# Performance work log

Measured on AMD Instinct MI355X. Metric: run time of the kernel, lower is better.

The kernel has to match this reference:

```python
import jax, jax.numpy as jnp
import numpy as np

N = 50000
E = 800000
D_IN = 128
D_H = 128
N_CLASSES = 40
N_HIDDEN = 2


def _gcn_norm(edge_index, num_nodes):
    # Add self loops, compute symmetric normalization D^-1/2 (A+I) D^-1/2
    loops = jnp.arange(num_nodes, dtype=edge_index.dtype)
    src = jnp.concatenate([edge_index[0], loops])
    dst = jnp.concatenate([edge_index[1], loops])
    deg = jax.ops.segment_sum(jnp.ones_like(src, dtype=jnp.float32), dst,
                              num_segments=num_nodes)
    dinv = jnp.where(deg > 0, jax.lax.rsqrt(jnp.maximum(deg, 1.0)), 0.0)
    norm = dinv[src] * dinv[dst]  # [E+N]
    return src, dst, norm


def _gcn_conv(x, src, dst, norm, W, b):
    h = x @ W                          # [N, d_out] transform first (PyG order)
    msg = h[src] * norm[:, None]       # gather + scale, [E+N, d_out]
    out = jax.ops.segment_sum(msg, dst, num_segments=x.shape[0])
    return out + b


def setup_inputs() -> dict:
    key = jax.random.key(0)
    ks = jax.random.split(key, 8)
    x = jax.random.normal(ks[0], (N, D_IN), dtype=jnp.float32)
    edge_index = jax.random.randint(ks[1], (2, E), 0, N, dtype=jnp.int64)
    s = 1.0 / np.sqrt(D_IN)
    W1 = jax.random.uniform(ks[2], (D_IN, D_H), minval=-s, maxval=s, dtype=jnp.float32)
    b1 = jnp.zeros((D_H,), dtype=jnp.float32)
    sh = 1.0 / np.sqrt(D_H)
    Wh = jax.random.uniform(ks[3], (N_HIDDEN, D_H, D_H), minval=-sh, maxval=sh, dtype=jnp.float32)
    bh = jnp.zeros((N_HIDDEN, D_H), dtype=jnp.float32)
    Wf = jax.random.uniform(ks[4], (D_H, N_CLASSES), minval=-sh, maxval=sh, dtype=jnp.float32)
    bf = jnp.zeros((N_CLASSES,), dtype=jnp.float32)
    return {"x": x, "edge_index": edge_index, "W1": W1, "b1": b1,
            "Wh": Wh, "bh": bh, "Wf": Wf, "bf": bf}


def reference(x, edge_index, W1, b1, Wh, bh, Wf, bf):
    src, dst, norm = _gcn_norm(edge_index, x.shape[0])
    h = jax.nn.relu(_gcn_conv(x, src, dst, norm, W1, b1))
    for i in range(Wh.shape[0]):  # small fixed layer count
        h = jax.nn.relu(_gcn_conv(h, src, dst, norm, Wh[i], bh[i]))
    # extra relu in original forward is a no-op after relu above
    return h @ Wf + bf
```

## Files before the change

### kernel.cpp

```cpp
#include <hip/hip_runtime.h>

#define D 128
#define NC 40

typedef __attribute__((ext_vector_type(8))) short short8v;
typedef __attribute__((ext_vector_type(4))) float f32x4;

__device__ __forceinline__ unsigned short f2bf(float f) {
    unsigned u = __float_as_uint(f);
    u += 0x7fff + ((u >> 16) & 1);
    return (unsigned short)(u >> 16);
}
__device__ __forceinline__ float bf2f(unsigned short h) {
    return __uint_as_float(((unsigned)h) << 16);
}

__device__ __forceinline__ int load_idx(const int* ei, long long pos, int is64) {
    return is64 ? ei[pos * 2] : ei[pos];
}

__device__ __forceinline__ int detect64(const int* __restrict__ ei) {
    int lane = threadIdx.x & 63;
    int hi = ei[lane * 2 + 1];
    return __any(hi != 0) ? 0 : 1;
}


__global__ void count_convert_kernel(const int* __restrict__ ei, int* __restrict__ deg,
                                     int E, int EB,
                                     const float* __restrict__ W1, const float* __restrict__ Wh,
                                     const float* __restrict__ Wf,
                                     unsigned short* __restrict__ Wc1, unsigned short* __restrict__ Wch0,
                                     unsigned short* __restrict__ Wch1, unsigned short* __restrict__ Wcf) {
    if (blockIdx.x < EB) {
        int is64 = detect64(ei);
        int e = blockIdx.x * 256 + threadIdx.x;
        if (e < E) {
            int d = load_idx(ei, (long long)E + e, is64);
            atomicAdd(&deg[d], 1);
        }
    } else {
        int idx = (blockIdx.x - EB) * 256 + threadIdx.x;
        if (idx < 49152) {
            int which = idx >> 14;
            int j = idx & 16383;
            int nn = j >> 7, k = j & 127;
            const float* W = (which == 0) ? W1 : (which == 1) ? Wh : Wh + 16384;
            unsigned short* o = (which == 0) ? Wc1 : (which == 1) ? Wch0 : Wch1;
            float v = W[k * 128 + nn];
            unsigned short h = f2bf(v);
            o[j] = h;
            o[16384 + j] = f2bf(v - bf2f(h));
        } else if (idx < 49152 + 6144) {
            int j = idx - 49152;
            int nn = j >> 7, k = j & 127;
            float v = (nn < NC) ? Wf[k * NC + nn] : 0.f;
            unsigned short h = f2bf(v);
            Wcf[j] = h;
            Wcf[6144 + j] = f2bf(v - bf2f(h));
        }
    }
}

__global__ void scan1_kernel(const int* __restrict__ deg, int* __restrict__ bsum, int m) {
    int i = blockIdx.x * 512 + threadIdx.x;
    int v = (i < m) ? deg[i] : 0;
    #pragma unroll
    for (int off = 32; off; off >>= 1) v += __shfl_down(v, off, 64);
    __shared__ int ws[8];
    if ((threadIdx.x & 63) == 0) ws[threadIdx.x >> 6] = v;
    __syncthreads();
    if (threadIdx.x == 0) {
        int s = 0;
        #pragma unroll
        for (int j = 0; j < 8; ++j) s += ws[j];
        bsum[blockIdx.x] = s;
    }
}

__global__ void scan3_kernel(const int* __restrict__ deg, const int* __restrict__ bsum,
                             int* __restrict__ rowptr, int* __restrict__ fill,
                             float* __restrict__ dinv, int n, int E, int nb) {
    int t = threadIdx.x;
    int lane = t & 63, w = t >> 6;
    int pv = (t < nb && t < (int)blockIdx.x) ? bsum[t] : 0;
    int rs = pv;
    #pragma unroll
    for (int off = 32; off; off >>= 1) rs += __shfl_down(rs, off, 64);
    __shared__ int red[8];
    if (lane == 0) red[w] = rs;
    __syncthreads();
    int base = 0;
    #pragma unroll
    for (int j = 0; j < 8; ++j) base += red[j];
    __syncthreads();

    int i = blockIdx.x * 512 + t;
    int v = (i < n) ? deg[i] : 0;
    int s = v;
    #pragma unroll
    for (int off = 1; off < 64; off <<= 1) {
        int x = __shfl_up(s, off, 64);
        if (lane >= off) s += x;
    }
    __shared__ int wsum[8];
    if (lane == 63) wsum[w] = s;
    __syncthreads();
    int wbase = 0;
    #pragma unroll
    for (int j = 0; j < 8; ++j) if (j < w) wbase += wsum[j];
    int excl = base + wbase + s - v;
    if (i < n) {
        rowptr[i] = excl;
        fill[i]   = excl;
        dinv[i]   = rsqrtf((float)(v + 1));
    }
    if (i == 0) rowptr[n] = E;
}

__global__ void scatter_kernel(const int* __restrict__ ei, int* __restrict__ fill,
                               const float* __restrict__ dinv, int2* __restrict__ col2, int E) {
    int is64 = detect64(ei);
    int e = blockIdx.x * 256 + threadIdx.x;
    if (e >= E) return;
    int s = load_idx(ei, (long long)e, is64);
    int d = load_idx(ei, (long long)E + e, is64);
    int pos = atomicAdd(&fill[d], 1);
    col2[pos] = make_int2(s, __float_as_int(dinv[s]));
}

__launch_bounds__(256)
__global__ void fused_wave_kernel(const float4* __restrict__ h4,
                                  const unsigned short* __restrict__ Wcvt,
                                  const float* __restrict__ bias,
                                  const float* __restrict__ dinv,
                                  const int* __restrict__ rowptr, const int2* __restrict__ col2,
                                  float* __restrict__ out, int n) {
    __shared__ unsigned short S[4][2][2][128];
    int t = threadIdx.x;
    int wv = t >> 6, l = t & 63;
    int p = l >> 5, li = l & 31;
    int kg = l >> 4, lr = l & 15;
    int base = blockIdx.x * 64 + wv * 16;
    if (base >= n) return;

    short8v fAh[4], fAl[4];
    #pragma unroll
    for (int ks = 0; ks < 4; ++ks) {
        fAh[ks] = (short8v){0,0,0,0,0,0,0,0};
        fAl[ks] = (short8v){0,0,0,0,0,0,0,0};
    }

    for (int j = 0; j < 8; ++j) {
        int node = base + 2 * j + p;
        int nd = (node < n) ? node : (n - 1);
        float dn = dinv[nd];
        size_t rowbase = (size_t)nd * 32;
        float4 hv = h4[rowbase + li];
        float4 acc;
        acc.x = hv.x * dn; acc.y = hv.y * dn; acc.z = hv.z * dn; acc.w = hv.w * dn;
        int e = rowptr[nd], e1 = rowptr[nd + 1];
        for (; e + 8 <= e1; e += 8) {
            int2 c[8];
            #pragma unroll
            for (int q = 0; q < 8; ++q) c[q] = col2[e + q];
            float4 v[8];
            #pragma unroll
            for (int q = 0; q < 8; ++q) v[q] = h4[(size_t)c[q].x * 32 + li];
            #pragma unroll
            for (int q = 0; q < 8; ++q) {
                float ds = __int_as_float(c[q].y);
                acc.x += v[q].x * ds; acc.y += v[q].y * ds;
                acc.z += v[q].z * ds; acc.w += v[q].w * ds;
            }
        }
        for (; e + 4 <= e1; e += 4) {
            int2 c[4];
            #pragma unroll
            for (int q = 0; q < 4; ++q) c[q] = col2[e + q];
            float4 v[4];
            #pragma unroll
            for (int q = 0; q < 4; ++q) v[q] = h4[(size_t)c[q].x * 32 + li];
            #pragma unroll
            for (int q = 0; q < 4; ++q) {
                float ds = __int_as_float(c[q].y);
                acc.x += v[q].x * ds; acc.y += v[q].y * ds;
                acc.z += v[q].z * ds; acc.w += v[q].w * ds;
            }
        }
        for (; e < e1; ++e) {
            int2 c = col2[e];
            float ds = __int_as_float(c.y);
            float4 v = h4[(size_t)c.x * 32 + li];
            acc.x += v.x * ds; acc.y += v.y * ds; acc.z += v.z * ds; acc.w += v.w * ds;
        }
        acc.x *= dn; acc.y *= dn; acc.z *= dn; acc.w *= dn;

        ushort4 hi, lo;
        hi.x = f2bf(acc.x); lo.x = f2bf(acc.x - bf2f(hi.x));
        hi.y = f2bf(acc.y); lo.y = f2bf(acc.y - bf2f(hi.y));
        hi.z = f2bf(acc.z); lo.z = f2bf(acc.z - bf2f(hi.z));
        hi.w = f2bf(acc.w); lo.w = f2bf(acc.w - bf2f(hi.w));
        *(ushort4*)&S[wv][0][p][li * 4] = hi;
        *(ushort4*)&S[wv][1][p][li * 4] = lo;
        __builtin_amdgcn_wave_barrier();
        if ((lr >> 1) == j) {
            int rp = lr & 1;
            #pragma unroll
            for (int ks = 0; ks < 4; ++ks) {
                fAh[ks] = *(short8v*)&S[wv][0][rp][ks * 32 + kg * 8];
                fAl[ks] = *(short8v*)&S[wv][1][rp][ks * 32 + kg * 8];
            }
        }
        __builtin_amdgcn_wave_barrier();
    }

    const unsigned short* Whi = Wcvt;
    const unsigned short* Wlo = Wcvt + 128 * 128;
    #pragma unroll
    for (int nt = 0; nt < 8; ++nt) {
        int col = nt * 16 + lr;
        short8v bh[4], bl[4];
        #pragma unroll
        for (int ks = 0; ks < 4; ++ks) {
            bh[ks] = *(const short8v*)&Whi[col * 128 + ks * 32 + kg * 8];
            bl[ks] = *(const short8v*)&Wlo[col * 128 + ks * 32 + kg * 8];
        }
        f32x4 o = (f32x4){0.f, 0.f, 0.f, 0.f};
        #pragma unroll
        for (int ks = 0; ks < 4; ++ks) {
            o = __builtin_amdgcn_mfma_f32_16x16x32_bf16(fAh[ks], bh[ks], o, 0, 0, 0);
            o = __builtin_amdgcn_mfma_f32_16x16x32_bf16(fAh[ks], bl[ks], o, 0, 0, 0);
            o = __builtin_amdgcn_mfma_f32_16x16x32_bf16(fAl[ks], bh[ks], o, 0, 0, 0);
        }
        float bv = bias[col];
        #pragma unroll
        for (int r = 0; r < 4; ++r) {
            int row = base + kg * 4 + r;
            if (row < n) out[(size_t)row * 128 + col] = fmaxf(o[r] + bv, 0.f);
        }
    }
}

__launch_bounds__(256)
__global__ void final_mfma_kernel(const float* __restrict__ A, const unsigned short* __restrict__ Wcvt,
                                  const float* __restrict__ bf, float* __restrict__ C, int M) {
    __shared__ unsigned short Ah[64 * 128];
    __shared__ unsigned short Al[64 * 128];
    int t = threadIdx.x;
    int l = t & 63, w = t >> 6;
    int lr = l & 15, lh = l >> 4;

    const unsigned short* Whi = Wcvt;
    const unsigned short* Wlo = Wcvt + 48 * 128;
    short8v bhi[3][4], blo[3][4];
    #pragma unroll
    for (int nt = 0; nt < 3; ++nt) {
        int n = nt * 16 + lr;
        #pragma unroll
        for (int ks = 0; ks < 4; ++ks) {
            bhi[nt][ks] = *(const short8v*)&Whi[n * 128 + ks * 32 + lh * 8];
            blo[nt][ks] = *(const short8v*)&Wlo[n * 128 + ks * 32 + lh * 8];
        }
    }

    int row0 = blockIdx.x * 64;
    #pragma unroll
    for (int c = 0; c < 4; ++c) {
        int chunk = c * 256 + t;
        int r  = chunk >> 4;
        int kc = chunk & 15;
        int gr = row0 + r; if (gr >= M) gr = M - 1;
        float4 a0 = *(const float4*)&A[(size_t)gr * 128 + kc * 8];
        float4 a1 = *(const float4*)&A[(size_t)gr * 128 + kc * 8 + 4];
        float av[8] = {a0.x, a0.y, a0.z, a0.w, a1.x, a1.y, a1.z, a1.w};
        short8v hv, lv;
        #pragma unroll
        for (int j = 0; j < 8; ++j) {
            unsigned short hi = f2bf(av[j]);
            hv[j] = (short)hi;
            lv[j] = (short)f2bf(av[j] - bf2f(hi));
        }
        int off = (r << 8) + ((kc << 4) ^ ((r & 7) << 4));
        *(short8v*)((char*)Ah + off) = hv;
        *(short8v*)((char*)Al + off) = lv;
    }
    __syncthreads();

    f32x4 acc[3];
    #pragma unroll
    for (int nt = 0; nt < 3; ++nt) acc[nt] = (f32x4){0.f, 0.f, 0.f, 0.f};
    int row = w * 16 + lr;
    #pragma unroll
    for (int ks = 0; ks < 4; ++ks) {
        int off = (row << 8) + (((ks << 6) + (lh << 4)) ^ ((row & 7) << 4));
        short8v ah = *(short8v*)((char*)Ah + off);
        short8v al = *(short8v*)((char*)Al + off);
        #pragma unroll
        for (int nt = 0; nt < 3; ++nt) {
            acc[nt] = __builtin_amdgcn_mfma_f32_16x16x32_bf16(ah, bhi[nt][ks], acc[nt], 0, 0, 0);
            acc[nt] = __builtin_amdgcn_mfma_f32_16x16x32_bf16(ah, blo[nt][ks], acc[nt], 0, 0, 0);
            acc[nt] = __builtin_amdgcn_mfma_f32_16x16x32_bf16(al, bhi[nt][ks], acc[nt], 0, 0, 0);
        }
    }
    #pragma unroll
    for (int nt = 0; nt < 3; ++nt) {
        int col = nt * 16 + lr;
        #pragma unroll
        for (int r = 0; r < 4; ++r) {
            int ro = row0 + w * 16 + lh * 4 + r;
            if (col < NC && ro < M) C[(size_t)ro * NC + col] = acc[nt][r] + bf[col];
        }
    }
}

extern "C" void kernel_launch(void* const* d_in, const int* in_sizes, int n_in,
                              void* d_out, int out_size, void* d_ws, size_t ws_size,
                              hipStream_t stream) {
    const float* x  = (const float*)d_in[0];
    const int*   ei = (const int*)d_in[1];
    const float* W1 = (const float*)d_in[2];
    const float* b1 = (const float*)d_in[3];
    const float* Wh = (const float*)d_in[4];
    const float* bh = (const float*)d_in[5];
    const float* Wf = (const float*)d_in[6];
    const float* bf = (const float*)d_in[7];
    float* out = (float*)d_out;

    int n = in_sizes[0] / D;
    int E = in_sizes[1] / 2;

    char* ws = (char*)d_ws;
    size_t off = 0;
    auto alloc = [&](size_t bytes) {
        void* p = ws + off;
        off = (off + bytes + 255) & ~(size_t)255;
        return p;
    };
    float* B0     = (float*)alloc((size_t)n * D * 4);
    float* B1     = (float*)alloc((size_t)n * D * 4);
    int*   deg    = (int*)alloc((size_t)n * 4);
    int*   rowptr = (int*)alloc((size_t)(n + 1) * 4);
    int*   fill   = (int*)alloc((size_t)n * 4);
    int2*  col2   = (int2*)alloc((size_t)E * 8);
    float* dinv   = (float*)alloc((size_t)n * 4);
    int*   bsum   = (int*)alloc(1024 * 4);
    unsigned short* Wc1  = (unsigned short*)alloc(2 * 128 * 128 * 2);
    unsigned short* Wch0 = (unsigned short*)alloc(2 * 128 * 128 * 2);
    unsigned short* Wch1 = (unsigned short*)alloc(2 * 128 * 128 * 2);
    unsigned short* Wcf  = (unsigned short*)alloc(2 * 48 * 128 * 2);

    int EB = (E + 255) / 256;
    int CB = (49152 + 6144 + 255) / 256;
    int nb = (n + 511) / 512;

    hipMemsetAsync(deg, 0, (size_t)n * 4, stream);
    count_convert_kernel<<<EB + CB, 256, 0, stream>>>(ei, deg, E, EB, W1, Wh, Wf, Wc1, Wch0, Wch1, Wcf);
    scan1_kernel<<<nb, 512, 0, stream>>>(deg, bsum, n);
    scan3_kernel<<<nb, 512, 0, stream>>>(deg, bsum, rowptr, fill, dinv, n, E, nb);
    scatter_kernel<<<EB, 256, 0, stream>>>(ei, fill, dinv, col2, E);

    int fgrid = (n + 63) / 64;

    fused_wave_kernel<<<fgrid, 256, 0, stream>>>((const float4*)x, Wc1, b1, dinv, rowptr, col2, B0, n);
    fused_wave_kernel<<<fgrid, 256, 0, stream>>>((const float4*)B0, Wch0, bh, dinv, rowptr, col2, B1, n);
    fused_wave_kernel<<<fgrid, 256, 0, stream>>>((const float4*)B1, Wch1, bh + D, dinv, rowptr, col2, B0, n);
    final_mfma_kernel<<<(n + 63) / 64, 256, 0, stream>>>(B0, Wcf, bf, out, n);
}
```

Measured before the change: 370.4 us.

## Use intra-block work stealing for GCN aggregation with shared-LDS MFMA transform

Replaces the per-wave fixed 16-node aggregation with a 512-thread block covering 32 nodes. Waves claim node pairs dynamically through a shared atomic counter, so uneven degrees are balanced across waves. Aggregated rows go into a swizzled LDS tile, and after a block barrier each of the 8 waves computes one 16-column slice of the 128x128 transform with bf16 split MFMA. The trade-off is extra atomics, a block-wide sync and smaller blocks, in exchange for better load balance and reuse of the weight fragments.

```diff
diff --git a/kernel.cpp b/kernel.cpp
--- a/kernel.cpp
+++ b/kernel.cpp
@@ -129,31 +129,30 @@
     col2[pos] = make_int2(s, __float_as_int(dinv[s]));
 }
 
-__launch_bounds__(256)
-__global__ void fused_wave_kernel(const float4* __restrict__ h4,
-                                  const unsigned short* __restrict__ Wcvt,
-                                  const float* __restrict__ bias,
-                                  const float* __restrict__ dinv,
-                                  const int* __restrict__ rowptr, const int2* __restrict__ col2,
-                                  float* __restrict__ out, int n) {
-    __shared__ unsigned short S[4][2][2][128];
+__launch_bounds__(512)
+__global__ void fused_steal_kernel(const float4* __restrict__ h4,
+                                   const unsigned short* __restrict__ Wcvt,
+                                   const float* __restrict__ bias,
+                                   const float* __restrict__ dinv,
+                                   const int* __restrict__ rowptr, const int2* __restrict__ col2,
+                                   float* __restrict__ out, int n) {
+    __shared__ unsigned short Ah[32 * 128];
+    __shared__ unsigned short Al[32 * 128];
+    __shared__ int pnodes[32];
+    __shared__ int cnt;
     int t = threadIdx.x;
     int wv = t >> 6, l = t & 63;
     int p = l >> 5, li = l & 31;
-    int kg = l >> 4, lr = l & 15;
-    int base = blockIdx.x * 64 + wv * 16;
-    if (base >= n) return;
-
-    short8v fAh[4], fAl[4];
-    #pragma unroll
-    for (int ks = 0; ks < 4; ++ks) {
-        fAh[ks] = (short8v){0,0,0,0,0,0,0,0};
-        fAl[ks] = (short8v){0,0,0,0,0,0,0,0};
-    }
-
-    for (int j = 0; j < 8; ++j) {
-        int node = base + 2 * j + p;
+    if (t == 0) cnt = 8;
+    __syncthreads();
+
+    int base = blockIdx.x * 32;
+    int pr = wv;
+    while (pr < 16) {
+        int row = 2 * pr + p;
+        int node = base + row;
         int nd = (node < n) ? node : (n - 1);
+        if (li == 0) pnodes[row] = (node < n) ? node : -1;
         float dn = dinv[nd];
         size_t rowbase = (size_t)nd * 32;
         float4 hv = h4[rowbase + li];
@@ -201,43 +200,45 @@
         hi.y = f2bf(acc.y); lo.y = f2bf(acc.y - bf2f(hi.y));
         hi.z = f2bf(acc.z); lo.z = f2bf(acc.z - bf2f(hi.z));
         hi.w = f2bf(acc.w); lo.w = f2bf(acc.w - bf2f(hi.w));
-        *(ushort4*)&S[wv][0][p][li * 4] = hi;
-        *(ushort4*)&S[wv][1][p][li * 4] = lo;
-        __builtin_amdgcn_wave_barrier();
-        if ((lr >> 1) == j) {
-            int rp = lr & 1;
-            #pragma unroll
-            for (int ks = 0; ks < 4; ++ks) {
-                fAh[ks] = *(short8v*)&S[wv][0][rp][ks * 32 + kg * 8];
-                fAl[ks] = *(short8v*)&S[wv][1][rp][ks * 32 + kg * 8];
-            }
-        }
-        __builtin_amdgcn_wave_barrier();
-    }
-
+        int off = (row << 8) + ((li << 3) ^ ((row & 7) << 4));
+        *(ushort4*)((char*)Ah + off) = hi;
+        *(ushort4*)((char*)Al + off) = lo;
+
+        int nxt;
+        if (l == 0) nxt = atomicAdd(&cnt, 1);
+        nxt = __shfl(nxt, 0);
+        pr = nxt;
+    }
+    __syncthreads();
+
+    int lr = l & 15, lh = l >> 4;
     const unsigned short* Whi = Wcvt;
     const unsigned short* Wlo = Wcvt + 128 * 128;
-    #pragma unroll
-    for (int nt = 0; nt < 8; ++nt) {
-        int col = nt * 16 + lr;
-        short8v bh[4], bl[4];
+    int col = wv * 16 + lr;
+    short8v bh[4], bl[4];
+    #pragma unroll
+    for (int ks = 0; ks < 4; ++ks) {
+        bh[ks] = *(const short8v*)&Whi[col * 128 + ks * 32 + lh * 8];
+        bl[ks] = *(const short8v*)&Wlo[col * 128 + ks * 32 + lh * 8];
+    }
+    float bv = bias[col];
+    #pragma unroll
+    for (int rt = 0; rt < 2; ++rt) {
+        f32x4 o = (f32x4){0.f, 0.f, 0.f, 0.f};
         #pragma unroll
         for (int ks = 0; ks < 4; ++ks) {
-            bh[ks] = *(const short8v*)&Whi[col * 128 + ks * 32 + kg * 8];
-            bl[ks] = *(const short8v*)&Wlo[col * 128 + ks * 32 + kg * 8];
-        }
-        f32x4 o = (f32x4){0.f, 0.f, 0.f, 0.f};
-        #pragma unroll
-        for (int ks = 0; ks < 4; ++ks) {
-            o = __builtin_amdgcn_mfma_f32_16x16x32_bf16(fAh[ks], bh[ks], o, 0, 0, 0);
-            o = __builtin_amdgcn_mfma_f32_16x16x32_bf16(fAh[ks], bl[ks], o, 0, 0, 0);
-            o = __builtin_amdgcn_mfma_f32_16x16x32_bf16(fAl[ks], bh[ks], o, 0, 0, 0);
-        }
-        float bv = bias[col];
+            int arow = rt * 16 + lr;
+            int aoff = (arow << 8) + (((ks << 6) + (lh << 4)) ^ ((arow & 7) << 4));
+            short8v ah = *(short8v*)((char*)Ah + aoff);
+            short8v al = *(short8v*)((char*)Al + aoff);
+            o = __builtin_amdgcn_mfma_f32_16x16x32_bf16(ah, bh[ks], o, 0, 0, 0);
+            o = __builtin_amdgcn_mfma_f32_16x16x32_bf16(ah, bl[ks], o, 0, 0, 0);
+            o = __builtin_amdgcn_mfma_f32_16x16x32_bf16(al, bh[ks], o, 0, 0, 0);
+        }
         #pragma unroll
         for (int r = 0; r < 4; ++r) {
-            int row = base + kg * 4 + r;
-            if (row < n) out[(size_t)row * 128 + col] = fmaxf(o[r] + bv, 0.f);
+            int prow = pnodes[rt * 16 + lh * 4 + r];
+            if (prow >= 0) out[(size_t)prow * 128 + col] = fmaxf(o[r] + bv, 0.f);
         }
     }
 }
@@ -360,10 +361,10 @@
     scan3_kernel<<<nb, 512, 0, stream>>>(deg, bsum, rowptr, fill, dinv, n, E, nb);
     scatter_kernel<<<EB, 256, 0, stream>>>(ei, fill, dinv, col2, E);
 
-    int fgrid = (n + 63) / 64;
-
-    fused_wave_kernel<<<fgrid, 256, 0, stream>>>((const float4*)x, Wc1, b1, dinv, rowptr, col2, B0, n);
-    fused_wave_kernel<<<fgrid, 256, 0, stream>>>((const float4*)B0, Wch0, bh, dinv, rowptr, col2, B1, n);
-    fused_wave_kernel<<<fgrid, 256, 0, stream>>>((const float4*)B1, Wch1, bh + D, dinv, rowptr, col2, B0, n);
+    int fgrid = (n + 31) / 32;
+
+    fused_steal_kernel<<<fgrid, 512, 0, stream>>>((const float4*)x, Wc1, b1, dinv, rowptr, col2, B0, n);
+    fused_steal_kernel<<<fgrid, 512, 0, stream>>>((const float4*)B0, Wch0, bh, dinv, rowptr, col2, B1, n);
+    fused_steal_kernel<<<fgrid, 512, 0, stream>>>((const float4*)B1, Wch1, bh + D, dinv, rowptr, col2, B0, n);
     final_mfma_kernel<<<(n + 63) / 64, 256, 0, stream>>>(B0, Wcf, bf, out, n);
 }
```

Result: faster. 326.1 us (-12.0%).

## Split fused layers into XCD-aware half-feature aggregation and separate MFMA transform

Applied to the files above, without the earlier changes.

Replaces each fused aggregate+GEMM kernel with two kernels. The first aggregates half the feature columns per node, with blocks mapped so that each group of four XCDs handles one column half. The aim is to shrink each XCD's working set of gathered rows and improve L2 hit rates. The second is a 64-row MFMA transform that stages A in shared memory, and the last layer's transform also fuses the final classifier GEMM. The cost is an extra round trip of the full aggregated feature matrix through global memory per layer, plus an added launch.

```diff
diff --git a/kernel.cpp b/kernel.cpp
--- a/kernel.cpp
+++ b/kernel.cpp
@@ -130,139 +130,76 @@
 }
 
 __launch_bounds__(256)
-__global__ void fused_wave_kernel(const float4* __restrict__ h4,
-                                  const unsigned short* __restrict__ Wcvt,
-                                  const float* __restrict__ bias,
-                                  const float* __restrict__ dinv,
-                                  const int* __restrict__ rowptr, const int2* __restrict__ col2,
-                                  float* __restrict__ out, int n) {
-    __shared__ unsigned short S[4][2][2][128];
-    int t = threadIdx.x;
-    int wv = t >> 6, l = t & 63;
-    int p = l >> 5, li = l & 31;
-    int kg = l >> 4, lr = l & 15;
-    int base = blockIdx.x * 64 + wv * 16;
-    if (base >= n) return;
-
-    short8v fAh[4], fAl[4];
-    #pragma unroll
-    for (int ks = 0; ks < 4; ++ks) {
-        fAh[ks] = (short8v){0,0,0,0,0,0,0,0};
-        fAl[ks] = (short8v){0,0,0,0,0,0,0,0};
-    }
-
-    for (int j = 0; j < 8; ++j) {
-        int node = base + 2 * j + p;
-        int nd = (node < n) ? node : (n - 1);
-        float dn = dinv[nd];
-        size_t rowbase = (size_t)nd * 32;
-        float4 hv = h4[rowbase + li];
-        float4 acc;
-        acc.x = hv.x * dn; acc.y = hv.y * dn; acc.z = hv.z * dn; acc.w = hv.w * dn;
-        int e = rowptr[nd], e1 = rowptr[nd + 1];
-        for (; e + 8 <= e1; e += 8) {
-            int2 c[8];
-            #pragma unroll
-            for (int q = 0; q < 8; ++q) c[q] = col2[e + q];
-            float4 v[8];
-            #pragma unroll
-            for (int q = 0; q < 8; ++q) v[q] = h4[(size_t)c[q].x * 32 + li];
-            #pragma unroll
-            for (int q = 0; q < 8; ++q) {
-                float ds = __int_as_float(c[q].y);
-                acc.x += v[q].x * ds; acc.y += v[q].y * ds;
-                acc.z += v[q].z * ds; acc.w += v[q].w * ds;
-            }
-        }
-        for (; e + 4 <= e1; e += 4) {
-            int2 c[4];
-            #pragma unroll
-            for (int q = 0; q < 4; ++q) c[q] = col2[e + q];
-            float4 v[4];
-            #pragma unroll
-            for (int q = 0; q < 4; ++q) v[q] = h4[(size_t)c[q].x * 32 + li];
-            #pragma unroll
-            for (int q = 0; q < 4; ++q) {
-                float ds = __int_as_float(c[q].y);
-                acc.x += v[q].x * ds; acc.y += v[q].y * ds;
-                acc.z += v[q].z * ds; acc.w += v[q].w * ds;
-            }
-        }
-        for (; e < e1; ++e) {
-            int2 c = col2[e];
-            float ds = __int_as_float(c.y);
-            float4 v = h4[(size_t)c.x * 32 + li];
-            acc.x += v.x * ds; acc.y += v.y * ds; acc.z += v.z * ds; acc.w += v.w * ds;
-        }
-        acc.x *= dn; acc.y *= dn; acc.z *= dn; acc.w *= dn;
-
-        ushort4 hi, lo;
-        hi.x = f2bf(acc.x); lo.x = f2bf(acc.x - bf2f(hi.x));
-        hi.y = f2bf(acc.y); lo.y = f2bf(acc.y - bf2f(hi.y));
-        hi.z = f2bf(acc.z); lo.z = f2bf(acc.z - bf2f(hi.z));
-        hi.w = f2bf(acc.w); lo.w = f2bf(acc.w - bf2f(hi.w));
-        *(ushort4*)&S[wv][0][p][li * 4] = hi;
-        *(ushort4*)&S[wv][1][p][li * 4] = lo;
-        __builtin_amdgcn_wave_barrier();
-        if ((lr >> 1) == j) {
-            int rp = lr & 1;
-            #pragma unroll
-            for (int ks = 0; ks < 4; ++ks) {
-                fAh[ks] = *(short8v*)&S[wv][0][rp][ks * 32 + kg * 8];
-                fAl[ks] = *(short8v*)&S[wv][1][rp][ks * 32 + kg * 8];
-            }
-        }
-        __builtin_amdgcn_wave_barrier();
-    }
-
-    const unsigned short* Whi = Wcvt;
-    const unsigned short* Wlo = Wcvt + 128 * 128;
-    #pragma unroll
-    for (int nt = 0; nt < 8; ++nt) {
-        int col = nt * 16 + lr;
-        short8v bh[4], bl[4];
-        #pragma unroll
-        for (int ks = 0; ks < 4; ++ks) {
-            bh[ks] = *(const short8v*)&Whi[col * 128 + ks * 32 + kg * 8];
-            bl[ks] = *(const short8v*)&Wlo[col * 128 + ks * 32 + kg * 8];
-        }
-        f32x4 o = (f32x4){0.f, 0.f, 0.f, 0.f};
-        #pragma unroll
-        for (int ks = 0; ks < 4; ++ks) {
-            o = __builtin_amdgcn_mfma_f32_16x16x32_bf16(fAh[ks], bh[ks], o, 0, 0, 0);
-            o = __builtin_amdgcn_mfma_f32_16x16x32_bf16(fAh[ks], bl[ks], o, 0, 0, 0);
-            o = __builtin_amdgcn_mfma_f32_16x16x32_bf16(fAl[ks], bh[ks], o, 0, 0, 0);
-        }
-        float bv = bias[col];
-        #pragma unroll
-        for (int r = 0; r < 4; ++r) {
-            int row = base + kg * 4 + r;
-            if (row < n) out[(size_t)row * 128 + col] = fmaxf(o[r] + bv, 0.f);
-        }
-    }
-}
-
+__global__ void agg_half_kernel(const float4* __restrict__ h4, const float* __restrict__ dinv,
+                                const int* __restrict__ rowptr, const int2* __restrict__ col2,
+                                float4* __restrict__ outA, int n, int T) {
+    int b = blockIdx.x;
+    int xcd = b & 7;
+    int half = xcd >> 2;
+    int tile = (b >> 3) * 4 + (xcd & 3);
+    if (tile >= T) return;
+    int g = threadIdx.x >> 4, li = threadIdx.x & 15;
+    int node = tile * 16 + g;
+    if (node >= n) return;
+    float dn = dinv[node];
+    size_t rowoff = (size_t)node * 32 + half * 16 + li;
+    float4 hv = h4[rowoff];
+    float4 acc;
+    acc.x = hv.x * dn; acc.y = hv.y * dn; acc.z = hv.z * dn; acc.w = hv.w * dn;
+    int e = rowptr[node], e1 = rowptr[node + 1];
+    int cbase = half * 16 + li;
+    for (; e + 8 <= e1; e += 8) {
+        int2 c[8];
+        #pragma unroll
+        for (int q = 0; q < 8; ++q) c[q] = col2[e + q];
+        float4 v[8];
+        #pragma unroll
+        for (int q = 0; q < 8; ++q) v[q] = h4[(size_t)c[q].x * 32 + cbase];
+        #pragma unroll
+        for (int q = 0; q < 8; ++q) {
+            float ds = __int_as_float(c[q].y);
+            acc.x += v[q].x * ds; acc.y += v[q].y * ds;
+            acc.z += v[q].z * ds; acc.w += v[q].w * ds;
+        }
+    }
+    for (; e + 4 <= e1; e += 4) {
+        int2 c[4];
+        #pragma unroll
+        for (int q = 0; q < 4; ++q) c[q] = col2[e + q];
+        float4 v[4];
+        #pragma unroll
+        for (int q = 0; q < 4; ++q) v[q] = h4[(size_t)c[q].x * 32 + cbase];
+        #pragma unroll
+        for (int q = 0; q < 4; ++q) {
+            float ds = __int_as_float(c[q].y);
+            acc.x += v[q].x * ds; acc.y += v[q].y * ds;
+            acc.z += v[q].z * ds; acc.w += v[q].w * ds;
+        }
+    }
+    for (; e < e1; ++e) {
+        int2 c = col2[e];
+        float ds = __int_as_float(c.y);
+        float4 v = h4[(size_t)c.x * 32 + cbase];
+        acc.x += v.x * ds; acc.y += v.y * ds; acc.z += v.z * ds; acc.w += v.w * ds;
+    }
+    acc.x *= dn; acc.y *= dn; acc.z *= dn; acc.w *= dn;
+    outA[rowoff] = acc;
+}
+
+template<int FINAL>
 __launch_bounds__(256)
-__global__ void final_mfma_kernel(const float* __restrict__ A, const unsigned short* __restrict__ Wcvt,
-                                  const float* __restrict__ bf, float* __restrict__ C, int M) {
+__global__ void transform_kernel(const float* __restrict__ A,
+                                 const unsigned short* __restrict__ Wcvt,
+                                 const float* __restrict__ bias,
+                                 float* __restrict__ out,
+                                 const unsigned short* __restrict__ Wfc,
+                                 const float* __restrict__ bf,
+                                 float* __restrict__ outF, int M) {
     __shared__ unsigned short Ah[64 * 128];
     __shared__ unsigned short Al[64 * 128];
     int t = threadIdx.x;
     int l = t & 63, w = t >> 6;
     int lr = l & 15, lh = l >> 4;
-
-    const unsigned short* Whi = Wcvt;
-    const unsigned short* Wlo = Wcvt + 48 * 128;
-    short8v bhi[3][4], blo[3][4];
-    #pragma unroll
-    for (int nt = 0; nt < 3; ++nt) {
-        int n = nt * 16 + lr;
-        #pragma unroll
-        for (int ks = 0; ks < 4; ++ks) {
-            bhi[nt][ks] = *(const short8v*)&Whi[n * 128 + ks * 32 + lh * 8];
-            blo[nt][ks] = *(const short8v*)&Wlo[n * 128 + ks * 32 + lh * 8];
-        }
-    }
 
     int row0 = blockIdx.x * 64;
     #pragma unroll
@@ -287,29 +224,108 @@
     }
     __syncthreads();
 
-    f32x4 acc[3];
-    #pragma unroll
-    for (int nt = 0; nt < 3; ++nt) acc[nt] = (f32x4){0.f, 0.f, 0.f, 0.f};
-    int row = w * 16 + lr;
-    #pragma unroll
-    for (int ks = 0; ks < 4; ++ks) {
-        int off = (row << 8) + (((ks << 6) + (lh << 4)) ^ ((row & 7) << 4));
-        short8v ah = *(short8v*)((char*)Ah + off);
-        short8v al = *(short8v*)((char*)Al + off);
+    const unsigned short* Whi = Wcvt;
+    const unsigned short* Wlo = Wcvt + 128 * 128;
+    short8v bh[2][4], bl[2][4];
+    int n0 = w * 32;
+    #pragma unroll
+    for (int ni = 0; ni < 2; ++ni) {
+        int nn = n0 + ni * 16 + lr;
+        #pragma unroll
+        for (int ks = 0; ks < 4; ++ks) {
+            bh[ni][ks] = *(const short8v*)&Whi[nn * 128 + ks * 32 + lh * 8];
+            bl[ni][ks] = *(const short8v*)&Wlo[nn * 128 + ks * 32 + lh * 8];
+        }
+    }
+
+    f32x4 acc[4][2];
+    #pragma unroll
+    for (int mi = 0; mi < 4; ++mi)
+        #pragma unroll
+        for (int ni = 0; ni < 2; ++ni)
+            acc[mi][ni] = (f32x4){0.f, 0.f, 0.f, 0.f};
+
+    #pragma unroll
+    for (int mi = 0; mi < 4; ++mi) {
+        int row = mi * 16 + lr;
+        #pragma unroll
+        for (int ks = 0; ks < 4; ++ks) {
+            int off = (row << 8) + (((ks << 6) + (lh << 4)) ^ ((row & 7) << 4));
+            short8v ah = *(short8v*)((char*)Ah + off);
+            short8v al = *(short8v*)((char*)Al + off);
+            #pragma unroll
+            for (int ni = 0; ni < 2; ++ni) {
+                acc[mi][ni] = __builtin_amdgcn_mfma_f32_16x16x32_bf16(ah, bh[ni][ks], acc[mi][ni], 0, 0, 0);
+                acc[mi][ni] = __builtin_amdgcn_mfma_f32_16x16x32_bf16(ah, bl[ni][ks], acc[mi][ni], 0, 0, 0);
+                acc[mi][ni] = __builtin_amdgcn_mfma_f32_16x16x32_bf16(al, bh[ni][ks], acc[mi][ni], 0, 0, 0);
+            }
+        }
+    }
+
+    if constexpr (!FINAL) {
+        #pragma unroll
+        for (int mi = 0; mi < 4; ++mi) {
+            #pragma unroll
+            for (int ni = 0; ni < 2; ++ni) {
+                float bv = bias[n0 + ni * 16 + lr];
+                #pragma unroll
+                for (int r = 0; r < 4; ++r) {
+                    int row = row0 + mi * 16 + lh * 4 + r;
+                    if (row < M)
+                        out[(size_t)row * 128 + n0 + ni * 16 + lr] = fmaxf(acc[mi][ni][r] + bv, 0.f);
+                }
+            }
+        }
+    } else {
+        __syncthreads();
+        #pragma unroll
+        for (int mi = 0; mi < 4; ++mi) {
+            #pragma unroll
+            for (int ni = 0; ni < 2; ++ni) {
+                float bv = bias[n0 + ni * 16 + lr];
+                int colc = n0 + ni * 16 + lr;
+                #pragma unroll
+                for (int r = 0; r < 4; ++r) {
+                    float v = fmaxf(acc[mi][ni][r] + bv, 0.f);
+                    unsigned short hv = f2bf(v);
+                    unsigned short lv = f2bf(v - bf2f(hv));
+                    int row = mi * 16 + lh * 4 + r;
+                    int boff = (row << 8) + ((2 * colc) ^ ((row & 7) << 4));
+                    *(unsigned short*)((char*)Ah + boff) = hv;
+                    *(unsigned short*)((char*)Al + boff) = lv;
+                }
+            }
+        }
+        __syncthreads();
+        const unsigned short* Fhi = Wfc;
+        const unsigned short* Flo = Wfc + 48 * 128;
         #pragma unroll
         for (int nt = 0; nt < 3; ++nt) {
-            acc[nt] = __builtin_amdgcn_mfma_f32_16x16x32_bf16(ah, bhi[nt][ks], acc[nt], 0, 0, 0);
-            acc[nt] = __builtin_amdgcn_mfma_f32_16x16x32_bf16(ah, blo[nt][ks], acc[nt], 0, 0, 0);
-            acc[nt] = __builtin_amdgcn_mfma_f32_16x16x32_bf16(al, bhi[nt][ks], acc[nt], 0, 0, 0);
-        }
-    }
-    #pragma unroll
-    for (int nt = 0; nt < 3; ++nt) {
-        int col = nt * 16 + lr;
-        #pragma unroll
-        for (int r = 0; r < 4; ++r) {
-            int ro = row0 + w * 16 + lh * 4 + r;
-            if (col < NC && ro < M) C[(size_t)ro * NC + col] = acc[nt][r] + bf[col];
+            int col48 = nt * 16 + lr;
+            short8v fh[4], fl[4];
+            #pragma unroll
+            for (int ks = 0; ks < 4; ++ks) {
+                fh[ks] = *(const short8v*)&Fhi[col48 * 128 + ks * 32 + lh * 8];
+                fl[ks] = *(const short8v*)&Flo[col48 * 128 + ks * 32 + lh * 8];
+            }
+            f32x4 of = (f32x4){0.f, 0.f, 0.f, 0.f};
+            #pragma unroll
+            for (int ks = 0; ks < 4; ++ks) {
+                int arow = w * 16 + lr;
+                int aoff = (arow << 8) + (((ks << 6) + (lh << 4)) ^ ((arow & 7) << 4));
+                short8v ah = *(short8v*)((char*)Ah + aoff);
+                short8v al = *(short8v*)((char*)Al + aoff);
+                of = __builtin_amdgcn_mfma_f32_16x16x32_bf16(ah, fh[ks], of, 0, 0, 0);
+                of = __builtin_amdgcn_mfma_f32_16x16x32_bf16(ah, fl[ks], of, 0, 0, 0);
+                of = __builtin_amdgcn_mfma_f32_16x16x32_bf16(al, fh[ks], of, 0, 0, 0);
+            }
+            float bfv = (col48 < NC) ? bf[col48] : 0.f;
+            #pragma unroll
+            for (int r = 0; r < 4; ++r) {
+                int ro = row0 + w * 16 + lh * 4 + r;
+                if (col48 < NC && ro < M)
+                    outF[(size_t)ro * NC + col48] = of[r] + bfv;
+            }
         }
     }
 }
@@ -339,6 +355,7 @@
     };
     float* B0     = (float*)alloc((size_t)n * D * 4);
     float* B1     = (float*)alloc((size_t)n * D * 4);
+    float* Bagg   = (float*)alloc((size_t)n * D * 4);
     int*   deg    = (int*)alloc((size_t)n * 4);
     int*   rowptr = (int*)alloc((size_t)(n + 1) * 4);
     int*   fill   = (int*)alloc((size_t)n * 4);
@@ -360,10 +377,14 @@
     scan3_kernel<<<nb, 512, 0, stream>>>(deg, bsum, rowptr, fill, dinv, n, E, nb);
     scatter_kernel<<<EB, 256, 0, stream>>>(ei, fill, dinv, col2, E);
 
-    int fgrid = (n + 63) / 64;
-
-    fused_wave_kernel<<<fgrid, 256, 0, stream>>>((const float4*)x, Wc1, b1, dinv, rowptr, col2, B0, n);
-    fused_wave_kernel<<<fgrid, 256, 0, stream>>>((const float4*)B0, Wch0, bh, dinv, rowptr, col2, B1, n);
-    fused_wave_kernel<<<fgrid, 256, 0, stream>>>((const float4*)B1, Wch1, bh + D, dinv, rowptr, col2, B0, n);
-    final_mfma_kernel<<<(n + 63) / 64, 256, 0, stream>>>(B0, Wcf, bf, out, n);
-}
+    int T = (n + 15) / 16;
+    int agrid = ((T + 3) / 4) * 8;
+    int tgrid = (n + 63) / 64;
+
+    agg_half_kernel<<<agrid, 256, 0, stream>>>((const float4*)x, dinv, rowptr, col2, (float4*)Bagg, n, T);
+    transform_kernel<0><<<tgrid, 256, 0, stream>>>(Bagg, Wc1, b1, B0, Wcf, bf, out, n);
+    agg_half_kernel<<<agrid, 256, 0, stream>>>((const float4*)B0, dinv, rowptr, col2, (float4*)Bagg, n, T);
+    transform_kernel<0><<<tgrid, 256, 0, stream>>>(Bagg, Wch0, bh, B1, Wcf, bf, out, n);
+    agg_half_kernel<<<agrid, 256, 0, stream>>>((const float4*)B1, dinv, rowptr, col2, (float4*)Bagg, n, T);
+    transform_kernel<1><<<tgrid, 256, 0, stream>>>(Bagg, Wch1, bh + D, B0, Wcf, bf, out, n);
+}
```

After: 317.4 us. -14.3%, faster.
